# Optimization experiments

Hardware: AMD Instinct MI355X
Metric: run time of the kernel (lower is better)

Reference implementation:

```python
import jax, jax.numpy as jnp
import numpy as np

N = 50000      # nodes
E = 800000     # edges (avg degree 16)
F_IN = 128
HID = 128
C = 40
EPS = 1e-5     # BatchNorm1d eps


def setup_inputs() -> dict:
    key = jax.random.key(0)
    ks = jax.random.split(key, 8)

    def glorot(k, shape):
        lim = np.sqrt(6.0 / (shape[0] + shape[1])).astype(np.float32)
        return jax.random.uniform(k, shape, jnp.float32, -lim, lim)

    inp = {
        "features": jax.random.normal(ks[0], (N, F_IN), jnp.float32),
        "edge_index": jax.random.randint(ks[1], (2, E), 0, N, jnp.int32),
        "W1": glorot(ks[2], (F_IN, HID)), "b1": jnp.zeros((HID,), jnp.float32),
        "gamma1": jnp.ones((HID,), jnp.float32), "beta1": jnp.zeros((HID,), jnp.float32),
        "W2": glorot(ks[3], (HID, HID)), "b2": jnp.zeros((HID,), jnp.float32),
        "gamma2": jnp.ones((HID,), jnp.float32), "beta2": jnp.zeros((HID,), jnp.float32),
        "W3": glorot(ks[4], (HID, C)), "b3": jnp.zeros((C,), jnp.float32),
    }
    return inp


def _gcn_norm(edge_index):
    # Add self-loops and compute symmetric normalization D^-1/2 (A+I) D^-1/2
    loops = jnp.arange(N, dtype=edge_index.dtype)
    src = jnp.concatenate([edge_index[0], loops])
    dst = jnp.concatenate([edge_index[1], loops])
    deg = jax.ops.segment_sum(jnp.ones((E + N,), jnp.float32), dst, num_segments=N)
    dinv = jax.lax.rsqrt(jnp.maximum(deg, 1.0))
    return src, dst, dinv[src] * dinv[dst]  # per-edge norm coefficient


def _gcn_conv(x, W, b, src, dst, norm):
    h = x @ W                                   # [N, out]
    msg = h[src] * norm[:, None]                # gather + scale, [E+N, out]
    return jax.ops.segment_sum(msg, dst, num_segments=N) + b


def _bn(x, gamma, beta):
    # training-mode BatchNorm1d over the node axis (biased variance)
    mu = jnp.mean(x, axis=0)
    var = jnp.mean(jnp.square(x - mu), axis=0)
    return (x - mu) * jax.lax.rsqrt(var + EPS) * gamma + beta


def reference(features, edge_index, W1, b1, gamma1, beta1, W2, b2, gamma2, beta2, W3, b3):
    src, dst, norm = _gcn_norm(edge_index)
    h = jax.nn.relu(_bn(_gcn_conv(features, W1, b1, src, dst, norm), gamma1, beta1))
    h = jax.nn.relu(_bn(_gcn_conv(h, W2, b2, src, dst, norm), gamma2, beta2))
    h = _gcn_conv(h, W3, b3, src, dst, norm)
    return jax.nn.log_softmax(h, axis=-1)
```

## Files before the change

kernel.cpp:

```cpp
#include <hip/hip_runtime.h>
#include <math.h>

#define FEAT 128
#define NCLS 40
#define BN_EPS 1e-5f

typedef unsigned short u16;
typedef unsigned int u32;
typedef __attribute__((ext_vector_type(8))) short bf16x8;
typedef __attribute__((ext_vector_type(4))) float f32x4;

__device__ inline u32 f2b2(float a, float b) {
    u32 ua = __float_as_uint(a), ub = __float_as_uint(b);
    ua = (ua + 0x7fffu + ((ua >> 16) & 1u)) >> 16;
    ub = (ub + 0x7fffu + ((ub >> 16) & 1u)) >> 16;
    return ua | (ub << 16);
}
__device__ inline u16 f2b1(float a) {
    u32 ua = __float_as_uint(a);
    return (u16)((ua + 0x7fffu + ((ua >> 16) & 1u)) >> 16);
}
__device__ inline float b2f(u16 u) { return __uint_as_float((u32)u << 16); }
__device__ inline float4 b4fv(ushort4 u) {
    return make_float4(b2f(u.x), b2f(u.y), b2f(u.z), b2f(u.w));
}
__device__ inline float blo(u32 u) { return __uint_as_float(u << 16); }
__device__ inline float bhi(u32 u) { return __uint_as_float(u & 0xffff0000u); }

__device__ inline void b8acc(uint4 u, float w, float* a) {
    a[0] = fmaf(w, blo(u.x), a[0]); a[1] = fmaf(w, bhi(u.x), a[1]);
    a[2] = fmaf(w, blo(u.y), a[2]); a[3] = fmaf(w, bhi(u.y), a[3]);
    a[4] = fmaf(w, blo(u.z), a[4]); a[5] = fmaf(w, bhi(u.z), a[5]);
    a[6] = fmaf(w, blo(u.w), a[6]); a[7] = fmaf(w, bhi(u.w), a[7]);
}

#define WT_PITCH 136
#define SMEM_BYTES (128 * WT_PITCH * 2)


__device__ inline void stage_wt(const float* __restrict__ W, u16* Wt) {
    const float4* W4 = (const float4*)W;
#pragma unroll
    for (int i = 0; i < 16; ++i) {
        int li = threadIdx.x + i * 256;
        int k = li >> 5;
        int n0 = (li & 31) * 4;
        float4 w = W4[li];
        Wt[(n0 + 0) * WT_PITCH + ((k + ((n0 + 0 & 3) << 5)) & 127)] = f2b1(w.x);
        Wt[(n0 + 1) * WT_PITCH + ((k + ((n0 + 1 & 3) << 5)) & 127)] = f2b1(w.y);
        Wt[(n0 + 2) * WT_PITCH + ((k + ((n0 + 2 & 3) << 5)) & 127)] = f2b1(w.z);
        Wt[(n0 + 3) * WT_PITCH + ((k + ((n0 + 3 & 3) << 5)) & 127)] = f2b1(w.w);
    }
}

__device__ inline void mfma_core(const u16* Wt, const bf16x8* bfrag,
                                 u16* __restrict__ Y, int node, int M, int nl, int quad) {
    f32x4 acc[8];
#pragma unroll
    for (int nt = 0; nt < 8; ++nt) acc[nt] = (f32x4){0.f, 0.f, 0.f, 0.f};
#pragma unroll
    for (int s = 0; s < 4; ++s) {
#pragma unroll
        for (int nt = 0; nt < 8; ++nt) {
            int nrow = nt * 16 + nl;
            int kk = ((s * 32 + quad * 8) + ((nl & 3) << 5)) & 127;
            uint4 aw = *(const uint4*)&Wt[nrow * WT_PITCH + kk];
            bf16x8 af = *(bf16x8*)&aw;
            acc[nt] = __builtin_amdgcn_mfma_f32_16x16x32_bf16(af, bfrag[s], acc[nt], 0, 0, 0);
        }
    }
    if (node < M) {
#pragma unroll
        for (int nt = 0; nt < 8; ++nt) {
            uint2 o;
            o.x = f2b2(acc[nt][0], acc[nt][1]);
            o.y = f2b2(acc[nt][2], acc[nt][3]);
            *(uint2*)&Y[(size_t)node * 128 + nt * 16 + quad * 4] = o;
        }
    }
}


__global__ __launch_bounds__(256) void k_l1_hist(
    const float* __restrict__ X, const float* __restrict__ W, u16* __restrict__ Y, int M,
    const int* __restrict__ dst, int* __restrict__ cnt, int E, int gemmBlocks)
{
    __shared__ __align__(16) char smem[SMEM_BYTES];

    if ((int)blockIdx.x < gemmBlocks) {
        u16* Wt = (u16*)smem;
        stage_wt(W, Wt);
        __syncthreads();

        int wv = threadIdx.x >> 6;
        int lane = threadIdx.x & 63;
        int nl = lane & 15, quad = lane >> 4;
        int node = blockIdx.x * 64 + wv * 16 + nl;

        bf16x8 bfrag[4];
        if (node < M) {
            const float4* xr = (const float4*)(X + (size_t)node * 128);
#pragma unroll
            for (int s = 0; s < 4; ++s) {
                float4 xa = xr[s * 8 + quad * 2];
                float4 xb = xr[s * 8 + quad * 2 + 1];
                uint4 bu;
                bu.x = f2b2(xa.x, xa.y); bu.y = f2b2(xa.z, xa.w);
                bu.z = f2b2(xb.x, xb.y); bu.w = f2b2(xb.z, xb.w);
                bfrag[s] = *(bf16x8*)&bu;
            }
        } else {
            uint4 z = make_uint4(0, 0, 0, 0);
#pragma unroll
            for (int s = 0; s < 4; ++s) bfrag[s] = *(bf16x8*)&z;
        }
        mfma_core(Wt, bfrag, Y, node, M, nl, quad);
    } else {
        int* lc = (int*)smem;
        int hb = blockIdx.x - gemmBlocks;
        int part = hb & 7;
        int chunk = hb >> 3;
        int lo = (int)(((long long)M * part) >> 3);
        int hi = (int)(((long long)M * (part + 1)) >> 3);
        int range = hi - lo;
        for (int i = threadIdx.x; i < range; i += 256) lc[i] = 0;
        __syncthreads();
        int per = (E + 63) / 64;
        int e0 = chunk * per;
        int e1 = e0 + per; if (e1 > E) e1 = E;
        for (int e = e0 + threadIdx.x; e < e1; e += 256) {
            int d = dst[e];
            if (d >= lo && d < hi) atomicAdd(&lc[d - lo], 1);
        }
        __syncthreads();
        for (int i = threadIdx.x; i < range; i += 256) {
            int v = lc[i];
            if (v) atomicAdd(&cnt[lo + i], v);
        }
    }
}


__global__ void k_scan_a(const int* __restrict__ cnt, int* __restrict__ bsum, int n) {
    int t = threadIdx.x;
    int idx = blockIdx.x * 512 + t * 2;
    int v = 0;
    if (idx < n) v += cnt[idx];
    if (idx + 1 < n) v += cnt[idx + 1];
    for (int d = 1; d < 64; d <<= 1) v += __shfl_xor(v, d, 64);
    __shared__ int ws[4];
    int lane = t & 63, w = t >> 6;
    if (lane == 0) ws[w] = v;
    __syncthreads();
    if (t == 0) bsum[blockIdx.x] = ws[0] + ws[1] + ws[2] + ws[3];
}

__global__ void k_scan_b(const int* __restrict__ bsum, int* __restrict__ boff,
                         int* __restrict__ row_off, int nb, int n) {
    if (threadIdx.x == 0) {
        int run = 0;
        for (int i = 0; i < nb; ++i) { boff[i] = run; run += bsum[i]; }
        row_off[n] = run;
    }
}

__global__ void k_scan_c(const int* __restrict__ cnt, const int* __restrict__ boff,
                         int* __restrict__ row_off, int* __restrict__ cursor,
                         float* __restrict__ dinv, int n) {
    int t = threadIdx.x;
    int idx = blockIdx.x * 512 + t * 2;
    int v0 = (idx < n) ? cnt[idx] : 0;
    int v1 = (idx + 1 < n) ? cnt[idx + 1] : 0;
    int s = v0 + v1;
    int lane = t & 63, w = t >> 6;
    int incl = s;
    for (int d = 1; d < 64; d <<= 1) {
        int o = __shfl_up(incl, d, 64);
        if (lane >= d) incl += o;
    }
    __shared__ int wsum[4];
    if (lane == 63) wsum[w] = incl;
    __syncthreads();
    int wpre = 0;
    for (int i = 0; i < w; ++i) wpre += wsum[i];
    int base = boff[blockIdx.x] + wpre + incl - s;
    if (idx < n) {
        row_off[idx] = base; cursor[idx] = base;
        dinv[idx] = rsqrtf((float)(v0 + 1));
    }
    if (idx + 1 < n) {
        row_off[idx + 1] = base + v0; cursor[idx + 1] = base + v0;
        dinv[idx + 1] = rsqrtf((float)(v1 + 1));
    }
}

__global__ __launch_bounds__(256) void k_fill(
    const int* __restrict__ src, const int* __restrict__ dst,
    int* __restrict__ cursor, int* __restrict__ col, float* __restrict__ wsrc,
    const float* __restrict__ dinv, int E, int n, int nchunks)
{
    int part = blockIdx.x & 7;
    int chunk = blockIdx.x >> 3;
    int lo = (int)(((long long)n * part) >> 3);
    int hi = (int)(((long long)n * (part + 1)) >> 3);
    int per = (E + nchunks - 1) / nchunks;
    int e0 = chunk * per;
    int e1 = e0 + per; if (e1 > E) e1 = E;
    for (int e = e0 + threadIdx.x; e < e1; e += 256) {
        int d = dst[e];
        if (d >= lo && d < hi) {
            int s = src[e];
            int p = atomicAdd(&cursor[d], 1);
            col[p] = s;
            wsrc[p] = dinv[s];
        }
    }
}


__global__ __launch_bounds__(256) void k_mfma_l2(
    const u16* __restrict__ X, const float* __restrict__ W,
    const float* __restrict__ sums, const float* __restrict__ gamma,
    const float* __restrict__ beta, u16* __restrict__ Y, int M)
{
    __shared__ __align__(16) u16 Wt[128 * WT_PITCH];
    __shared__ __align__(16) float scs[128], shs[128];

    if (threadIdx.x < 128) {
        int f = threadIdx.x;
        float inv_n = 1.f / (float)M;
        float mu = sums[f] * inv_n;
        float var = sums[128 + f] * inv_n - mu * mu;
        float rs = rsqrtf(var + BN_EPS);
        float sc = gamma[f] * rs;
        scs[f] = sc;
        shs[f] = beta[f] - mu * sc;
    }
    stage_wt(W, Wt);
    __syncthreads();

    int wv = threadIdx.x >> 6;
    int lane = threadIdx.x & 63;
    int nl = lane & 15, quad = lane >> 4;
    int node = blockIdx.x * 64 + wv * 16 + nl;

    bf16x8 bfrag[4];
    if (node < M) {
        const uint4* xr = (const uint4*)(X + (size_t)node * 128);
#pragma unroll
        for (int s = 0; s < 4; ++s) {
            int k0 = s * 32 + quad * 8;
            uint4 xu = xr[s * 4 + quad];
            float4 sc0 = *(const float4*)&scs[k0];
            float4 sc1 = *(const float4*)&scs[k0 + 4];
            float4 sh0 = *(const float4*)&shs[k0];
            float4 sh1 = *(const float4*)&shs[k0 + 4];
            float v0 = fmaxf(fmaf(blo(xu.x), sc0.x, sh0.x), 0.f);
            float v1 = fmaxf(fmaf(bhi(xu.x), sc0.y, sh0.y), 0.f);
            float v2 = fmaxf(fmaf(blo(xu.y), sc0.z, sh0.z), 0.f);
            float v3 = fmaxf(fmaf(bhi(xu.y), sc0.w, sh0.w), 0.f);
            float v4 = fmaxf(fmaf(blo(xu.z), sc1.x, sh1.x), 0.f);
            float v5 = fmaxf(fmaf(bhi(xu.z), sc1.y, sh1.y), 0.f);
            float v6 = fmaxf(fmaf(blo(xu.w), sc1.z, sh1.z), 0.f);
            float v7 = fmaxf(fmaf(bhi(xu.w), sc1.w, sh1.w), 0.f);
            uint4 bu;
            bu.x = f2b2(v0, v1); bu.y = f2b2(v2, v3);
            bu.z = f2b2(v4, v5); bu.w = f2b2(v6, v7);
            bfrag[s] = *(bf16x8*)&bu;
        }
    } else {
        uint4 z = make_uint4(0, 0, 0, 0);
#pragma unroll
        for (int s = 0; s < 4; ++s) bfrag[s] = *(bf16x8*)&z;
    }
    mfma_core(Wt, bfrag, Y, node, M, nl, quad);
}


__global__ __launch_bounds__(256) void k_gemm40(
    const u16* __restrict__ X, const float* __restrict__ W,
    const float* __restrict__ sums, const float* __restrict__ gamma,
    const float* __restrict__ beta, u16* __restrict__ Y, int M)
{
    __shared__ float Ws[128 * 40];
    __shared__ __align__(16) float scs[128], shs[128];
    __shared__ float Xs[32 * 260];

    int t = threadIdx.x;
    int row0 = blockIdx.x * 256;
    int tx = t & 3, ty = t >> 2;

    if (t < 128) {
        float inv_n = 1.f / (float)M;
        float mu = sums[t] * inv_n;
        float var = sums[128 + t] * inv_n - mu * mu;
        float rs = rsqrtf(var + BN_EPS);
        float sc = gamma[t] * rs;
        scs[t] = sc;
        shs[t] = beta[t] - mu * sc;
    }
    {
        const float4* W4 = (const float4*)W;
        float4* Ws4 = (float4*)Ws;
#pragma unroll
        for (int i = 0; i < 5; ++i) Ws4[t + i * 256] = W4[t + i * 256];
    }

    float acc[4][10];
#pragma unroll
    for (int r = 0; r < 4; ++r)
#pragma unroll
        for (int c = 0; c < 10; ++c) acc[r][c] = 0.f;

    for (int k0 = 0; k0 < 128; k0 += 32) {
        __syncthreads();
        {
            int rr = t >> 3;
            int kc = (t & 7) * 4;
            float4 sc = *(const float4*)&scs[k0 + kc];
            float4 sh = *(const float4*)&shs[k0 + kc];
#pragma unroll
            for (int p = 0; p < 8; ++p) {
                int r = rr + p * 32;
                int grow = row0 + r;
                float4 v = make_float4(0.f, 0.f, 0.f, 0.f);
                if (grow < M) v = b4fv(*(const ushort4*)(X + (size_t)grow * 128 + k0 + kc));
                v.x = fmaxf(fmaf(v.x, sc.x, sh.x), 0.f);
                v.y = fmaxf(fmaf(v.y, sc.y, sh.y), 0.f);
                v.z = fmaxf(fmaf(v.z, sc.z, sh.z), 0.f);
                v.w = fmaxf(fmaf(v.w, sc.w, sh.w), 0.f);
                Xs[(kc + 0) * 260 + r] = v.x;
                Xs[(kc + 1) * 260 + r] = v.y;
                Xs[(kc + 2) * 260 + r] = v.z;
                Xs[(kc + 3) * 260 + r] = v.w;
            }
        }
        __syncthreads();
#pragma unroll 8
        for (int kk = 0; kk < 32; ++kk) {
            const float4 xv = *(const float4*)&Xs[kk * 260 + ty * 4];
            const float xr[4] = {xv.x, xv.y, xv.z, xv.w};
            float wc[10];
#pragma unroll
            for (int c = 0; c < 5; ++c) {
                float2 w2 = *(const float2*)&Ws[(k0 + kk) * 40 + tx * 10 + c * 2];
                wc[c * 2] = w2.x; wc[c * 2 + 1] = w2.y;
            }
#pragma unroll
            for (int r = 0; r < 4; ++r)
#pragma unroll
                for (int c = 0; c < 10; ++c)
                    acc[r][c] = fmaf(xr[r], wc[c], acc[r][c]);
        }
    }

#pragma unroll
    for (int r = 0; r < 4; ++r) {
        int grow = row0 + ty * 4 + r;
        if (grow < M) {
            u32* yp = (u32*)(Y + (size_t)grow * 40 + tx * 10);
#pragma unroll
            for (int c = 0; c < 5; ++c)
                yp[c] = f2b2(acc[r][c * 2], acc[r][c * 2 + 1]);
        }
    }
}


__global__ __launch_bounds__(256) void k_agg128(
    const u16* __restrict__ t, const int* __restrict__ roff,
    const int* __restrict__ col, const float* __restrict__ wsrc,
    const float* __restrict__ dinv, const float* __restrict__ bias,
    u16* __restrict__ out, int n)
{
    int wid = threadIdx.x >> 4;
    int lane = threadIdx.x & 15;
    int i = blockIdx.x * 16 + wid;
    if (i >= n) return;
    int beg = roff[i], end = roff[i + 1];
    float di = dinv[i];

    float a[8];
    {
        uint4 su = ((const uint4*)(t + (size_t)i * 128))[lane];
        a[0] = di * blo(su.x); a[1] = di * bhi(su.x);
        a[2] = di * blo(su.y); a[3] = di * bhi(su.y);
        a[4] = di * blo(su.z); a[5] = di * bhi(su.z);
        a[6] = di * blo(su.w); a[7] = di * bhi(su.w);
    }

    int j = beg;
    for (; j + 7 < end; j += 8) {
        int s[8]; float w[8]; uint4 v[8];
#pragma unroll
        for (int k = 0; k < 8; ++k) { s[k] = col[j + k]; w[k] = wsrc[j + k]; }
#pragma unroll
        for (int k = 0; k < 8; ++k) v[k] = ((const uint4*)(t + (size_t)s[k] * 128))[lane];
#pragma unroll
        for (int k = 0; k < 8; ++k) b8acc(v[k], w[k], a);
    }
    for (; j < end; ++j) {
        float w0 = wsrc[j];
        uint4 v = ((const uint4*)(t + (size_t)col[j] * 128))[lane];
        b8acc(v, w0, a);
    }

    float4 bA = ((const float4*)bias)[lane * 2];
    float4 bB = ((const float4*)bias)[lane * 2 + 1];
    uint4 o;
    o.x = f2b2(fmaf(di, a[0], bA.x), fmaf(di, a[1], bA.y));
    o.y = f2b2(fmaf(di, a[2], bA.z), fmaf(di, a[3], bA.w));
    o.z = f2b2(fmaf(di, a[4], bB.x), fmaf(di, a[5], bB.y));
    o.w = f2b2(fmaf(di, a[6], bB.z), fmaf(di, a[7], bB.w));
    ((uint4*)(out + (size_t)i * 128))[lane] = o;
}


__global__ __launch_bounds__(256) void k_bnstats(const u16* __restrict__ a,
                                                 float* __restrict__ sums, int n) {
    int lane = threadIdx.x & 15;
    int rt = threadIdx.x >> 4;
    float s[8], q[8];
#pragma unroll
    for (int k = 0; k < 8; ++k) { s[k] = 0.f; q[k] = 0.f; }

    for (int i = blockIdx.x * 16 + rt; i < n; i += gridDim.x * 16) {
        uint4 u = ((const uint4*)(a + (size_t)i * 128))[lane];
        float v[8] = {blo(u.x), bhi(u.x), blo(u.y), bhi(u.y),
                      blo(u.z), bhi(u.z), blo(u.w), bhi(u.w)};
#pragma unroll
        for (int k = 0; k < 8; ++k) { s[k] += v[k]; q[k] = fmaf(v[k], v[k], q[k]); }
    }

    __shared__ float red[16][128];
#pragma unroll
    for (int k = 0; k < 8; ++k) red[rt][lane * 8 + k] = s[k];
    __syncthreads();
    if (threadIdx.x < 128) {
        float v = 0.f;
#pragma unroll
        for (int w = 0; w < 16; ++w) v += red[w][threadIdx.x];
        atomicAdd(&sums[threadIdx.x], v);
    }
    __syncthreads();
#pragma unroll
    for (int k = 0; k < 8; ++k) red[rt][lane * 8 + k] = q[k];
    __syncthreads();
    if (threadIdx.x < 128) {
        float v = 0.f;
#pragma unroll
        for (int w = 0; w < 16; ++w) v += red[w][threadIdx.x];
        atomicAdd(&sums[128 + threadIdx.x], v);
    }
}


__global__ __launch_bounds__(256) void k_agg40(
    const u16* __restrict__ t, const int* __restrict__ roff,
    const int* __restrict__ col, const float* __restrict__ wsrc,
    const float* __restrict__ dinv, const float* __restrict__ bias,
    float* __restrict__ out, int n)
{
    int i = blockIdx.x * 32 + (threadIdx.x >> 3);
    if (i >= n) return;
    int l = threadIdx.x & 7;
    bool act = l < 5;
    int beg = roff[i], end = roff[i + 1];
    float di = dinv[i];

    float a[8] = {0.f, 0.f, 0.f, 0.f, 0.f, 0.f, 0.f, 0.f};
    if (act) {
        uint4 su = ((const uint4*)(t + (size_t)i * NCLS))[l];
        a[0] = di * blo(su.x); a[1] = di * bhi(su.x);
        a[2] = di * blo(su.y); a[3] = di * bhi(su.y);
        a[4] = di * blo(su.z); a[5] = di * bhi(su.z);
        a[6] = di * blo(su.w); a[7] = di * bhi(su.w);
    }
    int j = beg;
    for (; j + 7 < end; j += 8) {
        int s[8]; float w[8]; uint4 v[8];
#pragma unroll
        for (int k = 0; k < 8; ++k) { s[k] = col[j + k]; w[k] = wsrc[j + k]; }
#pragma unroll
        for (int k = 0; k < 8; ++k)
            v[k] = act ? ((const uint4*)(t + (size_t)s[k] * NCLS))[l]
                       : make_uint4(0, 0, 0, 0);
#pragma unroll
        for (int k = 0; k < 8; ++k) b8acc(v[k], w[k], a);
    }
    for (; j < end; ++j) {
        float w0 = wsrc[j];
        uint4 v = act ? ((const uint4*)(t + (size_t)col[j] * NCLS))[l]
                      : make_uint4(0, 0, 0, 0);
        b8acc(v, w0, a);
    }

    float v[8];
    float m = -INFINITY;
    if (act) {
        float4 b0 = *(const float4*)(bias + l * 8);
        float4 b1 = *(const float4*)(bias + l * 8 + 4);
        v[0] = fmaf(di, a[0], b0.x); v[1] = fmaf(di, a[1], b0.y);
        v[2] = fmaf(di, a[2], b0.z); v[3] = fmaf(di, a[3], b0.w);
        v[4] = fmaf(di, a[4], b1.x); v[5] = fmaf(di, a[5], b1.y);
        v[6] = fmaf(di, a[6], b1.z); v[7] = fmaf(di, a[7], b1.w);
#pragma unroll
        for (int k = 0; k < 8; ++k) m = fmaxf(m, v[k]);
    }
#pragma unroll
    for (int d = 1; d < 8; d <<= 1) m = fmaxf(m, __shfl_xor(m, d, 8));
    float es = 0.f;
    if (act) {
#pragma unroll
        for (int k = 0; k < 8; ++k) es += expf(v[k] - m);
    }
#pragma unroll
    for (int d = 1; d < 8; d <<= 1) es += __shfl_xor(es, d, 8);
    float ls = logf(es);
    if (act) {
        float4 o0, o1;
        o0.x = v[0] - m - ls; o0.y = v[1] - m - ls;
        o0.z = v[2] - m - ls; o0.w = v[3] - m - ls;
        o1.x = v[4] - m - ls; o1.y = v[5] - m - ls;
        o1.z = v[6] - m - ls; o1.w = v[7] - m - ls;
        *(float4*)(out + (size_t)i * NCLS + l * 8) = o0;
        *(float4*)(out + (size_t)i * NCLS + l * 8 + 4) = o1;
    }
}


extern "C" void kernel_launch(void* const* d_in, const int* in_sizes, int n_in,
                              void* d_out, int out_size, void* d_ws, size_t ws_size,
                              hipStream_t stream) {
    const float* features = (const float*)d_in[0];
    const int* edge_index = (const int*)d_in[1];
    const float* W1 = (const float*)d_in[2];
    const float* b1 = (const float*)d_in[3];
    const float* gamma1 = (const float*)d_in[4];
    const float* beta1 = (const float*)d_in[5];
    const float* W2 = (const float*)d_in[6];
    const float* b2 = (const float*)d_in[7];
    const float* gamma2 = (const float*)d_in[8];
    const float* beta2 = (const float*)d_in[9];
    const float* W3 = (const float*)d_in[10];
    const float* b3 = (const float*)d_in[11];
    float* out = (float*)d_out;

    int n = in_sizes[0] / FEAT;
    int E = in_sizes[1] / 2;

    char* p = (char*)d_ws;
    auto alloc = [&](size_t bytes) -> void* {
        void* r = (void*)p;
        p += (bytes + 255) & ~(size_t)255;
        return r;
    };
    int* cnt     = (int*)alloc((size_t)n * 4);
    int* row_off = (int*)alloc((size_t)(n + 1) * 4);
    int* cursor  = (int*)alloc((size_t)n * 4);
    int* colb    = (int*)alloc((size_t)E * 4);
    float* wsrc  = (float*)alloc((size_t)E * 4);
    int* bsum    = (int*)alloc(1024);
    int* boff    = (int*)alloc(1024);
    float* dinv  = (float*)alloc((size_t)n * 4);
    float* sums  = (float*)alloc(256 * 4);
    u16* hb      = (u16*)alloc((size_t)n * 128 * 2);
    u16* ab      = (u16*)alloc((size_t)n * 128 * 2);

    const int* e_src = edge_index;
    const int* e_dst = edge_index + E;

    int gb64 = (n + 63) / 64;
    int gb16 = (n + 15) / 16;
    int gb32 = (n + 31) / 32;
    int nb = (n + 511) / 512;

    hipMemsetAsync(cnt, 0, (size_t)n * 4, stream);
    k_l1_hist<<<gb64 + 512, 256, 0, stream>>>(features, W1, hb, n, e_dst, cnt, E, gb64);
    k_scan_a<<<nb, 256, 0, stream>>>(cnt, bsum, n);
    k_scan_b<<<1, 64, 0, stream>>>(bsum, boff, row_off, nb, n);
    k_scan_c<<<nb, 256, 0, stream>>>(cnt, boff, row_off, cursor, dinv, n);
    int nchunks = 160;
    k_fill<<<nchunks * 8, 256, 0, stream>>>(e_src, e_dst, cursor, colb, wsrc, dinv, E, n, nchunks);

    k_agg128<<<gb16, 256, 0, stream>>>(hb, row_off, colb, wsrc, dinv, b1, ab, n);
    hipMemsetAsync(sums, 0, 256 * 4, stream);
    k_bnstats<<<512, 256, 0, stream>>>(ab, sums, n);

    k_mfma_l2<<<gb64, 256, 0, stream>>>(ab, W2, sums, gamma1, beta1, hb, n);
    k_agg128<<<gb16, 256, 0, stream>>>(hb, row_off, colb, wsrc, dinv, b2, ab, n);
    hipMemsetAsync(sums, 0, 256 * 4, stream);
    k_bnstats<<<512, 256, 0, stream>>>(ab, sums, n);

    k_gemm40<<<(n + 255) / 256, 256, 0, stream>>>(ab, W3, sums, gamma2, beta2, hb, n);
    k_agg40<<<gb32, 256, 0, stream>>>(hb, row_off, colb, wsrc, dinv, b3, out, n);
}
```

Baseline: 359.5 us.

## Fuse BatchNorm statistics into aggregation and use global atomics for degree histogram

Each 128-wide aggregation kernel now reduces per-column sums and squared sums of its fp32 outputs in shared memory and atomically adds them to a per-layer stats buffer, removing the separate bnstats kernels that re-read the activations. Both stats buffers are zeroed by one memset up front. The histogram part of the layer-1 kernel drops the partitioned shared-memory histogram and does one global atomicAdd per edge over a grid-stride loop. The fused path adds about 3125 blocks × 256 global float atomics per layer, and stats now come from fp32 values instead of the bf16-rounded stored outputs.

```diff
diff --git a/kernel.cpp b/kernel.cpp
--- a/kernel.cpp
+++ b/kernel.cpp
@@ -35,7 +35,6 @@
 }
 
 #define WT_PITCH 136
-#define SMEM_BYTES (128 * WT_PITCH * 2)
 
 
 __device__ inline void stage_wt(const float* __restrict__ W, u16* Wt) {
@@ -83,12 +82,12 @@
 
 __global__ __launch_bounds__(256) void k_l1_hist(
     const float* __restrict__ X, const float* __restrict__ W, u16* __restrict__ Y, int M,
-    const int* __restrict__ dst, int* __restrict__ cnt, int E, int gemmBlocks)
+    const int* __restrict__ dst, int* __restrict__ cnt, int E,
+    int gemmBlocks, int histBlocks)
 {
-    __shared__ __align__(16) char smem[SMEM_BYTES];
+    __shared__ __align__(16) u16 Wt[128 * WT_PITCH];
 
     if ((int)blockIdx.x < gemmBlocks) {
-        u16* Wt = (u16*)smem;
         stage_wt(W, Wt);
         __syncthreads();
 
@@ -116,27 +115,10 @@
         }
         mfma_core(Wt, bfrag, Y, node, M, nl, quad);
     } else {
-        int* lc = (int*)smem;
-        int hb = blockIdx.x - gemmBlocks;
-        int part = hb & 7;
-        int chunk = hb >> 3;
-        int lo = (int)(((long long)M * part) >> 3);
-        int hi = (int)(((long long)M * (part + 1)) >> 3);
-        int range = hi - lo;
-        for (int i = threadIdx.x; i < range; i += 256) lc[i] = 0;
-        __syncthreads();
-        int per = (E + 63) / 64;
-        int e0 = chunk * per;
-        int e1 = e0 + per; if (e1 > E) e1 = E;
-        for (int e = e0 + threadIdx.x; e < e1; e += 256) {
-            int d = dst[e];
-            if (d >= lo && d < hi) atomicAdd(&lc[d - lo], 1);
-        }
-        __syncthreads();
-        for (int i = threadIdx.x; i < range; i += 256) {
-            int v = lc[i];
-            if (v) atomicAdd(&cnt[lo + i], v);
-        }
+        int tb = blockIdx.x - gemmBlocks;
+        int stride = histBlocks * 256;
+        for (int e = tb * 256 + threadIdx.x; e < E; e += stride)
+            atomicAdd(&cnt[dst[e]], 1);
     }
 }
 
@@ -371,70 +353,59 @@
     const u16* __restrict__ t, const int* __restrict__ roff,
     const int* __restrict__ col, const float* __restrict__ wsrc,
     const float* __restrict__ dinv, const float* __restrict__ bias,
-    u16* __restrict__ out, int n)
+    u16* __restrict__ out, float* __restrict__ sums, int n)
 {
     int wid = threadIdx.x >> 4;
     int lane = threadIdx.x & 15;
     int i = blockIdx.x * 16 + wid;
-    if (i >= n) return;
-    int beg = roff[i], end = roff[i + 1];
-    float di = dinv[i];
-
-    float a[8];
-    {
-        uint4 su = ((const uint4*)(t + (size_t)i * 128))[lane];
-        a[0] = di * blo(su.x); a[1] = di * bhi(su.x);
-        a[2] = di * blo(su.y); a[3] = di * bhi(su.y);
-        a[4] = di * blo(su.z); a[5] = di * bhi(su.z);
-        a[6] = di * blo(su.w); a[7] = di * bhi(su.w);
-    }
-
-    int j = beg;
-    for (; j + 7 < end; j += 8) {
-        int s[8]; float w[8]; uint4 v[8];
-#pragma unroll
-        for (int k = 0; k < 8; ++k) { s[k] = col[j + k]; w[k] = wsrc[j + k]; }
-#pragma unroll
-        for (int k = 0; k < 8; ++k) v[k] = ((const uint4*)(t + (size_t)s[k] * 128))[lane];
-#pragma unroll
-        for (int k = 0; k < 8; ++k) b8acc(v[k], w[k], a);
-    }
-    for (; j < end; ++j) {
-        float w0 = wsrc[j];
-        uint4 v = ((const uint4*)(t + (size_t)col[j] * 128))[lane];
-        b8acc(v, w0, a);
-    }
-
-    float4 bA = ((const float4*)bias)[lane * 2];
-    float4 bB = ((const float4*)bias)[lane * 2 + 1];
-    uint4 o;
-    o.x = f2b2(fmaf(di, a[0], bA.x), fmaf(di, a[1], bA.y));
-    o.y = f2b2(fmaf(di, a[2], bA.z), fmaf(di, a[3], bA.w));
-    o.z = f2b2(fmaf(di, a[4], bB.x), fmaf(di, a[5], bB.y));
-    o.w = f2b2(fmaf(di, a[6], bB.z), fmaf(di, a[7], bB.w));
-    ((uint4*)(out + (size_t)i * 128))[lane] = o;
-}
-
-
-__global__ __launch_bounds__(256) void k_bnstats(const u16* __restrict__ a,
-                                                 float* __restrict__ sums, int n) {
-    int lane = threadIdx.x & 15;
-    int rt = threadIdx.x >> 4;
-    float s[8], q[8];
-#pragma unroll
-    for (int k = 0; k < 8; ++k) { s[k] = 0.f; q[k] = 0.f; }
-
-    for (int i = blockIdx.x * 16 + rt; i < n; i += gridDim.x * 16) {
-        uint4 u = ((const uint4*)(a + (size_t)i * 128))[lane];
-        float v[8] = {blo(u.x), bhi(u.x), blo(u.y), bhi(u.y),
-                      blo(u.z), bhi(u.z), blo(u.w), bhi(u.w)};
-#pragma unroll
-        for (int k = 0; k < 8; ++k) { s[k] += v[k]; q[k] = fmaf(v[k], v[k], q[k]); }
+
+    float o[8] = {0.f, 0.f, 0.f, 0.f, 0.f, 0.f, 0.f, 0.f};
+
+    if (i < n) {
+        int beg = roff[i], end = roff[i + 1];
+        float di = dinv[i];
+
+        float a[8];
+        {
+            uint4 su = ((const uint4*)(t + (size_t)i * 128))[lane];
+            a[0] = di * blo(su.x); a[1] = di * bhi(su.x);
+            a[2] = di * blo(su.y); a[3] = di * bhi(su.y);
+            a[4] = di * blo(su.z); a[5] = di * bhi(su.z);
+            a[6] = di * blo(su.w); a[7] = di * bhi(su.w);
+        }
+
+        int j = beg;
+        for (; j + 7 < end; j += 8) {
+            int s[8]; float w[8]; uint4 v[8];
+#pragma unroll
+            for (int k = 0; k < 8; ++k) { s[k] = col[j + k]; w[k] = wsrc[j + k]; }
+#pragma unroll
+            for (int k = 0; k < 8; ++k) v[k] = ((const uint4*)(t + (size_t)s[k] * 128))[lane];
+#pragma unroll
+            for (int k = 0; k < 8; ++k) b8acc(v[k], w[k], a);
+        }
+        for (; j < end; ++j) {
+            float w0 = wsrc[j];
+            uint4 v = ((const uint4*)(t + (size_t)col[j] * 128))[lane];
+            b8acc(v, w0, a);
+        }
+
+        float4 bA = ((const float4*)bias)[lane * 2];
+        float4 bB = ((const float4*)bias)[lane * 2 + 1];
+        o[0] = fmaf(di, a[0], bA.x); o[1] = fmaf(di, a[1], bA.y);
+        o[2] = fmaf(di, a[2], bA.z); o[3] = fmaf(di, a[3], bA.w);
+        o[4] = fmaf(di, a[4], bB.x); o[5] = fmaf(di, a[5], bB.y);
+        o[6] = fmaf(di, a[6], bB.z); o[7] = fmaf(di, a[7], bB.w);
+
+        uint4 ov;
+        ov.x = f2b2(o[0], o[1]); ov.y = f2b2(o[2], o[3]);
+        ov.z = f2b2(o[4], o[5]); ov.w = f2b2(o[6], o[7]);
+        ((uint4*)(out + (size_t)i * 128))[lane] = ov;
     }
 
     __shared__ float red[16][128];
 #pragma unroll
-    for (int k = 0; k < 8; ++k) red[rt][lane * 8 + k] = s[k];
+    for (int k = 0; k < 8; ++k) red[wid][lane * 8 + k] = o[k];
     __syncthreads();
     if (threadIdx.x < 128) {
         float v = 0.f;
@@ -444,7 +415,7 @@
     }
     __syncthreads();
 #pragma unroll
-    for (int k = 0; k < 8; ++k) red[rt][lane * 8 + k] = q[k];
+    for (int k = 0; k < 8; ++k) red[wid][lane * 8 + k] = o[k] * o[k];
     __syncthreads();
     if (threadIdx.x < 128) {
         float v = 0.f;
@@ -563,9 +534,12 @@
     int* bsum    = (int*)alloc(1024);
     int* boff    = (int*)alloc(1024);
     float* dinv  = (float*)alloc((size_t)n * 4);
-    float* sums  = (float*)alloc(256 * 4);
+    float* sums  = (float*)alloc(512 * 4);
     u16* hb      = (u16*)alloc((size_t)n * 128 * 2);
     u16* ab      = (u16*)alloc((size_t)n * 128 * 2);
+
+    float* sums1 = sums;
+    float* sums2 = sums + 256;
 
     const int* e_src = edge_index;
     const int* e_dst = edge_index + E;
@@ -576,22 +550,21 @@
     int nb = (n + 511) / 512;
 
     hipMemsetAsync(cnt, 0, (size_t)n * 4, stream);
-    k_l1_hist<<<gb64 + 512, 256, 0, stream>>>(features, W1, hb, n, e_dst, cnt, E, gb64);
+    hipMemsetAsync(sums, 0, 512 * 4, stream);
+    int histBlocks = 512;
+    k_l1_hist<<<gb64 + histBlocks, 256, 0, stream>>>(features, W1, hb, n,
+                                                     e_dst, cnt, E, gb64, histBlocks);
     k_scan_a<<<nb, 256, 0, stream>>>(cnt, bsum, n);
     k_scan_b<<<1, 64, 0, stream>>>(bsum, boff, row_off, nb, n);
     k_scan_c<<<nb, 256, 0, stream>>>(cnt, boff, row_off, cursor, dinv, n);
     int nchunks = 160;
     k_fill<<<nchunks * 8, 256, 0, stream>>>(e_src, e_dst, cursor, colb, wsrc, dinv, E, n, nchunks);
 
-    k_agg128<<<gb16, 256, 0, stream>>>(hb, row_off, colb, wsrc, dinv, b1, ab, n);
-    hipMemsetAsync(sums, 0, 256 * 4, stream);
-    k_bnstats<<<512, 256, 0, stream>>>(ab, sums, n);
-
-    k_mfma_l2<<<gb64, 256, 0, stream>>>(ab, W2, sums, gamma1, beta1, hb, n);
-    k_agg128<<<gb16, 256, 0, stream>>>(hb, row_off, colb, wsrc, dinv, b2, ab, n);
-    hipMemsetAsync(sums, 0, 256 * 4, stream);
-    k_bnstats<<<512, 256, 0, stream>>>(ab, sums, n);
-
-    k_gemm40<<<(n + 255) / 256, 256, 0, stream>>>(ab, W3, sums, gamma2, beta2, hb, n);
+    k_agg128<<<gb16, 256, 0, stream>>>(hb, row_off, colb, wsrc, dinv, b1, ab, sums1, n);
+
+    k_mfma_l2<<<gb64, 256, 0, stream>>>(ab, W2, sums1, gamma1, beta1, hb, n);
+    k_agg128<<<gb16, 256, 0, stream>>>(hb, row_off, colb, wsrc, dinv, b2, ab, sums2, n);
+
+    k_gemm40<<<(n + 255) / 256, 256, 0, stream>>>(ab, W3, sums2, gamma2, beta2, hb, n);
     k_agg40<<<gb32, 256, 0, stream>>>(hb, row_off, colb, wsrc, dinv, b3, out, n);
 }
```

After: 436.3 us. +21.4%, slower.
